# Kernel optimization log

Measured on AMD Instinct MI355X. Metric: run time of the kernel, lower is better.

The kernel has to match this reference:

```python
import jax, jax.numpy as jnp
import numpy as np
import math

EMBED_DIM = 2048
NUM_HEADS = 32
NUM_KV_HEADS = 8
HEAD_DIM = EMBED_DIM // NUM_HEADS  # 64
N_REP = NUM_HEADS // NUM_KV_HEADS  # 4
BATCH = 2
SEQ = 2048


def _rope_tables(seq_len, head_dim):
    # standard RoPE tables matching rotate_half convention (frequencies tiled twice)
    inv_freq = 1.0 / (10000.0 ** (np.arange(0, head_dim, 2, dtype=np.float32) / head_dim))
    t = np.arange(seq_len, dtype=np.float32)
    freqs = np.outer(t, inv_freq)                      # (seq, head_dim/2)
    emb = np.concatenate([freqs, freqs], axis=-1)      # (seq, head_dim)
    return jnp.asarray(np.cos(emb)), jnp.asarray(np.sin(emb))


def setup_inputs() -> dict:
    key = jax.random.key(0)
    ks = jax.random.split(key, 6)
    scale = 1.0 / math.sqrt(EMBED_DIM)
    x = jax.random.normal(ks[0], (BATCH, SEQ, EMBED_DIM), dtype=jnp.float32)
    wq = jax.random.normal(ks[1], (EMBED_DIM, EMBED_DIM), dtype=jnp.float32) * scale
    wk = jax.random.normal(ks[2], (NUM_KV_HEADS * HEAD_DIM, EMBED_DIM), dtype=jnp.float32) * scale
    wv = jax.random.normal(ks[3], (NUM_KV_HEADS * HEAD_DIM, EMBED_DIM), dtype=jnp.float32) * scale
    wo = jax.random.normal(ks[4], (EMBED_DIM, EMBED_DIM), dtype=jnp.float32) * scale
    freqs_cos, freqs_sin = _rope_tables(SEQ, HEAD_DIM)
    return {"x": x, "freqs_cos": freqs_cos, "freqs_sin": freqs_sin,
            "wq": wq, "wk": wk, "wv": wv, "wo": wo}


def _rotate_half(t):
    h = t.shape[-1] // 2
    return jnp.concatenate([-t[..., h:], t[..., :h]], axis=-1)


def reference(x, freqs_cos, freqs_sin, wq, wk, wv, wo):
    b, s, _ = x.shape
    # QKV projections (Linear with weight (out,in): y = x @ W^T)
    xq = (x @ wq.T).reshape(b, s, NUM_HEADS, HEAD_DIM).transpose(0, 2, 1, 3)     # (b,H,s,d)
    xk = (x @ wk.T).reshape(b, s, NUM_KV_HEADS, HEAD_DIM).transpose(0, 2, 1, 3)  # (b,Hkv,s,d)
    xv = (x @ wv.T).reshape(b, s, NUM_KV_HEADS, HEAD_DIM).transpose(0, 2, 1, 3)
    # RoPE: cos/sin (s,d) broadcast over (b,h,s,d)
    xq = xq * freqs_cos + _rotate_half(xq) * freqs_sin
    xk = xk * freqs_cos + _rotate_half(xk) * freqs_sin
    # GQA: repeat_interleave kv heads to match q heads
    xk = jnp.repeat(xk, N_REP, axis=1)  # (b,H,s,d)
    xv = jnp.repeat(xv, N_REP, axis=1)
    scores = jnp.einsum('bhqd,bhkd->bhqk', xq, xk) / math.sqrt(HEAD_DIM)
    causal = jnp.tril(jnp.ones((s, s), dtype=bool))
    scores = jnp.where(causal, scores, jnp.float32(-1e30))
    attn = jax.nn.softmax(scores, axis=-1)
    out = jnp.einsum('bhqk,bhkd->bhqd', attn, xv)        # (b,H,s,d)
    out = out.transpose(0, 2, 1, 3).reshape(b, s, EMBED_DIM)
    return out @ wo.T
```

## Files before the change

kernel.cpp:

```cpp
#include <hip/hip_runtime.h>

#define BATCH 2
#define SEQ 2048
#define EMBED 2048
#define NHEADS 32
#define NKV 8
#define HDIM 64
#define QKV_LD 3072
#define LOG2E 1.44269504088896f

typedef __attribute__((ext_vector_type(8))) short short8;
typedef __attribute__((ext_vector_type(4))) float f32x4;

__device__ inline float hw_exp2(float x) { return __builtin_amdgcn_exp2f(x); }

__device__ inline ushort f2bf(float f) {
  union { float f; unsigned u; } v{f};
  unsigned r = v.u + 0x7FFF + ((v.u >> 16) & 1);
  return (ushort)(r >> 16);
}
__device__ inline float bf2f(ushort u) {
  union { unsigned u; float f; } v{((unsigned)u) << 16};
  return v.f;
}
__device__ inline unsigned fbits(float f) {
  union { float f; unsigned u; } v{f};
  return v.u;
}

__device__ inline void gload16(const ushort* g, ushort* l) {
  __builtin_amdgcn_global_load_lds(
      (const __attribute__((address_space(1))) unsigned*)g,
      (__attribute__((address_space(3))) unsigned*)l, 16, 0, 0);
}

#define PHASE_BAR()                          \
  do {                                       \
    __builtin_amdgcn_sched_barrier(0);       \
    __builtin_amdgcn_s_barrier();            \
    __builtin_amdgcn_sched_barrier(0);       \
  } while (0)

__global__ __launch_bounds__(256) void cvt_all(const float* __restrict__ x,
                                               const float* __restrict__ wq,
                                               const float* __restrict__ wk,
                                               const float* __restrict__ wv,
                                               const float* __restrict__ wo,
                                               ushort* __restrict__ xb,
                                               ushort* __restrict__ wqkv,
                                               ushort* __restrict__ wob) {
  size_t e = (size_t)(blockIdx.x * blockDim.x + threadIdx.x) * 8;
  const float* src;
  ushort* dst;
  if (e < 8388608u) { src = x + e; dst = xb + e; }
  else if (e < 12582912u) { size_t o = e - 8388608u; src = wq + o; dst = wqkv + o; }
  else if (e < 13631488u) { size_t o = e - 12582912u; src = wk + o; dst = wqkv + 4194304u + o; }
  else if (e < 14680064u) { size_t o = e - 13631488u; src = wv + o; dst = wqkv + 5242880u + o; }
  else { size_t o = e - 14680064u; src = wo + o; dst = wob + o; }
  float4 v0 = ((const float4*)src)[0];
  float4 v1 = ((const float4*)src)[1];
  union { uint4 v; ushort u[8]; } pk;
  pk.u[0] = f2bf(v0.x); pk.u[1] = f2bf(v0.y); pk.u[2] = f2bf(v0.z); pk.u[3] = f2bf(v0.w);
  pk.u[4] = f2bf(v1.x); pk.u[5] = f2bf(v1.y); pk.u[6] = f2bf(v1.z); pk.u[7] = f2bf(v1.w);
  *(uint4*)dst = pk.v;
}

template <int BN, typename OutT>
__global__ __launch_bounds__(512) void gemm8p(const ushort* __restrict__ Ag,
                                              const ushort* __restrict__ Bg,
                                              OutT* __restrict__ C,
                                              int M, int N, int K) {
  constexpr int NF = BN / 64;
  __shared__ ushort As[2][2][256][32];
  __shared__ ushort Bs[2][2][BN][32];
  const int tid = threadIdx.x;
  const int lane = tid & 63, wave = tid >> 6;
  const int quad = lane >> 4, l16 = lane & 15;
  const int wm = wave >> 2, wn = wave & 3;
  const int m0 = blockIdx.y * 256, n0 = blockIdx.x * BN;
  const int NT = K >> 6;

  auto stA = [&](int Tn, int h) {
    const int r0 = h * 128 + wave * 16;
    const ushort* g = Ag + (size_t)(m0 + r0 + (lane >> 2)) * K + Tn * 64 + (lane & 3) * 8;
    gload16(g, &As[Tn & 1][0][r0][0]);
    gload16(g + 32, &As[Tn & 1][1][r0][0]);
  };
  auto stB = [&](int Tn, int h) {
    const int r0 = h * 128 + wave * 16;
    const ushort* g = Bg + (size_t)(n0 + r0 + (lane >> 2)) * K + Tn * 64 + (lane & 3) * 8;
    gload16(g, &Bs[Tn & 1][0][r0][0]);
    gload16(g + 32, &Bs[Tn & 1][1][r0][0]);
  };

  f32x4 acc[8][NF] = {};

  stA(0, 0); stA(0, 1);
  stB(0, 0);
  if constexpr (BN == 256) stB(0, 1);

  for (int T = 0; T < NT; ++T) {
    const int bf = T & 1;
    asm volatile("s_waitcnt vmcnt(0)" ::: "memory");
    PHASE_BAR();

    short8 bfr[NF][2];
#pragma unroll
    for (int nf = 0; nf < NF; nf++)
#pragma unroll
      for (int kk = 0; kk < 2; kk++)
        bfr[nf][kk] = *(short8*)&Bs[bf][kk][wn * (16 * NF) + nf * 16 + l16][quad * 8];

#pragma unroll
    for (int q = 0; q < 4; q++) {
      short8 afr[2][2];
#pragma unroll
      for (int mq = 0; mq < 2; mq++)
#pragma unroll
        for (int kk = 0; kk < 2; kk++)
          afr[mq][kk] = *(short8*)&As[bf][kk][wm * 128 + (2 * q + mq) * 16 + l16][quad * 8];

      if (T + 1 < NT) {
        if (q == 0) stA(T + 1, 0);
        else if (q == 1) stA(T + 1, 1);
        else if (q == 2) stB(T + 1, 0);
        else if constexpr (BN == 256) stB(T + 1, 1);
      }

      __builtin_amdgcn_s_setprio(1);
#pragma unroll
      for (int mq = 0; mq < 2; mq++)
#pragma unroll
        for (int nf = 0; nf < NF; nf++)
#pragma unroll
          for (int kk = 0; kk < 2; kk++)
            acc[2 * q + mq][nf] = __builtin_amdgcn_mfma_f32_16x16x32_bf16(
                afr[mq][kk], bfr[nf][kk], acc[2 * q + mq][nf], 0, 0, 0);
      __builtin_amdgcn_s_setprio(0);
      PHASE_BAR();
    }
  }

#pragma unroll
  for (int mf = 0; mf < 8; mf++) {
#pragma unroll
    for (int r = 0; r < 4; r++) {
      size_t rg = (size_t)(m0 + wm * 128 + mf * 16 + quad * 4 + r);
#pragma unroll
      for (int nf = 0; nf < NF; nf++) {
        int cg = n0 + wn * (16 * NF) + nf * 16 + l16;
        if constexpr (sizeof(OutT) == 2)
          C[rg * N + cg] = f2bf(acc[mf][nf][r]);
        else
          C[rg * N + cg] = acc[mf][nf][r];
      }
    }
  }
}

__global__ __launch_bounds__(256) void rope_qk(ushort* __restrict__ t,
                                               const float* __restrict__ fc,
                                               const float* __restrict__ fs,
                                               int total) {
  int idx = blockIdx.x * blockDim.x + threadIdx.x;
  if (idx >= total) return;
  int g = idx & 3;
  int hh = (idx >> 2) % 40;
  int tok = idx / 160;
  int s = tok & (SEQ - 1);
  float scale = (hh < 32) ? 0.125f * LOG2E : 1.0f;
  ushort* p = t + (size_t)tok * QKV_LD + hh * 64 + g * 8;
  union { uint4 v; ushort u[8]; } lo, hi, olo, ohi;
  lo.v = *(const uint4*)p;
  hi.v = *(const uint4*)(p + 32);
  const float* fcb = fc + s * HDIM + g * 8;
  const float* fsb = fs + s * HDIM + g * 8;
  float4 c0a = ((const float4*)fcb)[0], c0b = ((const float4*)fcb)[1];
  float4 s0a = ((const float4*)fsb)[0], s0b = ((const float4*)fsb)[1];
  float4 c1a = ((const float4*)(fcb + 32))[0], c1b = ((const float4*)(fcb + 32))[1];
  float4 s1a = ((const float4*)(fsb + 32))[0], s1b = ((const float4*)(fsb + 32))[1];
  float cc0[8] = {c0a.x, c0a.y, c0a.z, c0a.w, c0b.x, c0b.y, c0b.z, c0b.w};
  float ss0[8] = {s0a.x, s0a.y, s0a.z, s0a.w, s0b.x, s0b.y, s0b.z, s0b.w};
  float cc1[8] = {c1a.x, c1a.y, c1a.z, c1a.w, c1b.x, c1b.y, c1b.z, c1b.w};
  float ss1[8] = {s1a.x, s1a.y, s1a.z, s1a.w, s1b.x, s1b.y, s1b.z, s1b.w};
#pragma unroll
  for (int j = 0; j < 8; j++) {
    float x0 = bf2f(lo.u[j]), x1 = bf2f(hi.u[j]);
    olo.u[j] = f2bf((x0 * cc0[j] - x1 * ss0[j]) * scale);
    ohi.u[j] = f2bf((x1 * cc1[j] + x0 * ss1[j]) * scale);
  }
  *(uint4*)p = olo.v;
  *(uint4*)(p + 32) = ohi.v;
}

__global__ __launch_bounds__(256, 4) void attn_mfma(const ushort* __restrict__ QKV,
                                                    ushort* __restrict__ O) {
  __shared__ ushort Ks[64][72];
  __shared__ ushort Vt[64][72];
  __shared__ ushort Pw[4][16][72];
  const int tid = threadIdx.x;
  const int lane = tid & 63, wave = tid >> 6;
  const int quad = lane >> 4, l16 = lane & 15;

  const int bid = blockIdx.x;
  const int qq = bid >> 8;
  const int j4 = (bid >> 6) & 3;
  const int bh = bid & 63;
  const int qblk = (qq >> 1) * 8 + ((qq & 1) ? 7 - j4 : j4);

  const int b = bh >> 5, h = bh & 31, kh = h >> 2;
  const int ntiles = 2 * qblk + 2;
  const int wrow = qblk * 128 + wave * 32;

  short8 qf[2][2];
#pragma unroll
  for (int f = 0; f < 2; f++)
#pragma unroll
    for (int c = 0; c < 2; c++)
      qf[f][c] = *(const short8*)(QKV +
          (size_t)(b * SEQ + wrow + f * 16 + l16) * QKV_LD +
          h * HDIM + c * 32 + quad * 8);

  f32x4 o[2][4] = {};
  float m[2] = {-INFINITY, -INFINITY}, l[2] = {0.f, 0.f};

  const ushort* Kbase = QKV + (size_t)b * SEQ * QKV_LD + 2048 + kh * HDIM;
  const ushort* Vbase = Kbase + 512;
  const int kp = tid & 31, dg = tid >> 5;

  for (int t = 0; t < ntiles; t++) {
    const int k0 = t * 64;
    __syncthreads();
    {
      const float4* kpp = (const float4*)(Kbase + (size_t)(k0 + lane) * QKV_LD + wave * 16);
      float4 kv0 = kpp[0], kv1 = kpp[1];
      const uint4* va4 = (const uint4*)(Vbase + (size_t)(k0 + 2 * kp) * QKV_LD + dg * 8);
      const uint4* vb4 = (const uint4*)(Vbase + (size_t)(k0 + 2 * kp + 1) * QKV_LD + dg * 8);
      uint4 va = va4[0], vb = vb4[0];
      *(float4*)&Ks[lane][wave * 16] = kv0;
      *(float4*)&Ks[lane][wave * 16 + 8] = kv1;
      const unsigned* vaw = (const unsigned*)&va;
      const unsigned* vbw = (const unsigned*)&vb;
#pragma unroll
      for (int j = 0; j < 8; j++) {
        unsigned pk = (j & 1)
            ? __builtin_amdgcn_perm(vbw[j >> 1], vaw[j >> 1], 0x07060302)
            : __builtin_amdgcn_perm(vbw[j >> 1], vaw[j >> 1], 0x05040100);
        *(unsigned*)&Vt[dg * 8 + j][2 * kp] = pk;
      }
    }
    __syncthreads();

    if (k0 > wrow + 31) continue;
    const bool a0 = (k0 <= wrow + 15);

    f32x4 s0[4], s1[4];
    __builtin_amdgcn_s_setprio(1);
#pragma unroll
    for (int nt = 0; nt < 4; nt++) {
      short8 kf0 = *(short8*)&Ks[nt * 16 + l16][quad * 8];
      short8 kf1 = *(short8*)&Ks[nt * 16 + l16][32 + quad * 8];
      f32x4 z1 = {};
      z1 = __builtin_amdgcn_mfma_f32_16x16x32_bf16(kf0, qf[1][0], z1, 0, 0, 0);
      s1[nt] = __builtin_amdgcn_mfma_f32_16x16x32_bf16(kf1, qf[1][1], z1, 0, 0, 0);
      if (a0) {
        f32x4 z0 = {};
        z0 = __builtin_amdgcn_mfma_f32_16x16x32_bf16(kf0, qf[0][0], z0, 0, 0, 0);
        s0[nt] = __builtin_amdgcn_mfma_f32_16x16x32_bf16(kf1, qf[0][1], z0, 0, 0, 0);
      }
    }
    __builtin_amdgcn_s_setprio(0);

    if (k0 + 63 > wrow + 16) {
      const int lim1 = wrow + 16 + l16 - k0;
#pragma unroll
      for (int nt = 0; nt < 4; nt++)
#pragma unroll
        for (int r = 0; r < 4; r++)
          if (nt * 16 + quad * 4 + r > lim1) s1[nt][r] = -INFINITY;
    }
    if (a0 && k0 + 63 > wrow) {
      const int lim0 = wrow + l16 - k0;
#pragma unroll
      for (int nt = 0; nt < 4; nt++)
#pragma unroll
        for (int r = 0; r < 4; r++)
          if (nt * 16 + quad * 4 + r > lim0) s0[nt][r] = -INFINITY;
    }

    auto smx = [&](f32x4 (&s)[4], float& mm, float& ll, f32x4 (&oo)[4]) {
      float mx = s[0][0];
#pragma unroll
      for (int nt = 0; nt < 4; nt++)
#pragma unroll
        for (int r = 0; r < 4; r++) mx = fmaxf(mx, s[nt][r]);
      mx = fmaxf(mx, __shfl_xor(mx, 16));
      mx = fmaxf(mx, __shfl_xor(mx, 32));
      if (!__all(mx <= mm + 8.f)) {
        float mnew = fmaxf(mm, mx);
        float al = hw_exp2(mm - mnew);
        mm = mnew;
        ll *= al;
#pragma unroll
        for (int dt = 0; dt < 4; dt++)
#pragma unroll
          for (int r = 0; r < 4; r++) oo[dt][r] *= al;
      }
      float psum = 0.f;
#pragma unroll
      for (int nt = 0; nt < 4; nt++) {
        float p0 = hw_exp2(s[nt][0] - mm), p1 = hw_exp2(s[nt][1] - mm);
        float p2 = hw_exp2(s[nt][2] - mm), p3 = hw_exp2(s[nt][3] - mm);
        psum += (p0 + p1) + (p2 + p3);
        unsigned lo = __builtin_amdgcn_perm(fbits(p1), fbits(p0), 0x07060302);
        unsigned hi = __builtin_amdgcn_perm(fbits(p3), fbits(p2), 0x07060302);
        uint2 pk; pk.x = lo; pk.y = hi;
        *(uint2*)&Pw[wave][l16][nt * 16 + quad * 4] = pk;
      }
      psum += __shfl_xor(psum, 16);
      psum += __shfl_xor(psum, 32);
      ll += psum;
    };

    short8 pf00, pf01, pf10, pf11;
    if (a0) {
      smx(s0, m[0], l[0], o[0]);
      pf00 = *(short8*)&Pw[wave][l16][quad * 8];
      pf01 = *(short8*)&Pw[wave][l16][32 + quad * 8];
    }
    smx(s1, m[1], l[1], o[1]);
    pf10 = *(short8*)&Pw[wave][l16][quad * 8];
    pf11 = *(short8*)&Pw[wave][l16][32 + quad * 8];

    __builtin_amdgcn_s_setprio(1);
#pragma unroll
    for (int dt = 0; dt < 4; dt++) {
      short8 vf0 = *(short8*)&Vt[dt * 16 + l16][quad * 8];
      short8 vf1 = *(short8*)&Vt[dt * 16 + l16][32 + quad * 8];
      o[1][dt] = __builtin_amdgcn_mfma_f32_16x16x32_bf16(vf0, pf10, o[1][dt], 0, 0, 0);
      o[1][dt] = __builtin_amdgcn_mfma_f32_16x16x32_bf16(vf1, pf11, o[1][dt], 0, 0, 0);
      if (a0) {
        o[0][dt] = __builtin_amdgcn_mfma_f32_16x16x32_bf16(vf0, pf00, o[0][dt], 0, 0, 0);
        o[0][dt] = __builtin_amdgcn_mfma_f32_16x16x32_bf16(vf1, pf01, o[0][dt], 0, 0, 0);
      }
    }
    __builtin_amdgcn_s_setprio(0);
  }

#pragma unroll
  for (int f = 0; f < 2; f++) {
    float inv = 1.0f / l[f];
    size_t rowg = (size_t)(b * SEQ + wrow + f * 16 + l16) * EMBED + h * HDIM;
#pragma unroll
    for (int dt = 0; dt < 4; dt++) {
      ushort q0 = f2bf(o[f][dt][0] * inv), q1 = f2bf(o[f][dt][1] * inv);
      ushort q2 = f2bf(o[f][dt][2] * inv), q3 = f2bf(o[f][dt][3] * inv);
      uint2 pk;
      pk.x = (unsigned)q0 | ((unsigned)q1 << 16);
      pk.y = (unsigned)q2 | ((unsigned)q3 << 16);
      *(uint2*)&O[rowg + dt * 16 + quad * 4] = pk;
    }
  }
}

extern "C" void kernel_launch(void* const* d_in, const int* in_sizes, int n_in,
                              void* d_out, int out_size, void* d_ws, size_t ws_size,
                              hipStream_t stream) {
  const float* x = (const float*)d_in[0];
  const float* fcos = (const float*)d_in[1];
  const float* fsin = (const float*)d_in[2];
  const float* wq = (const float*)d_in[3];
  const float* wk = (const float*)d_in[4];
  const float* wv = (const float*)d_in[5];
  const float* wo = (const float*)d_in[6];
  float* out = (float*)d_out;

  const int M = BATCH * SEQ;
  ushort* ws = (ushort*)d_ws;
  ushort* xb = ws;
  ushort* wqkv = xb + (size_t)M * EMBED;
  ushort* wob = wqkv + (size_t)QKV_LD * EMBED;
  ushort* QKVb = wob + (size_t)EMBED * EMBED;
  ushort* Ab = QKVb + (size_t)M * QKV_LD;

  dim3 blk(256);
  cvt_all<<<9216, blk, 0, stream>>>(x, wq, wk, wv, wo, xb, wqkv, wob);

  gemm8p<256, ushort><<<dim3(QKV_LD / 256, M / 256), dim3(512), 0, stream>>>(xb, wqkv, QKVb, M, QKV_LD, EMBED);

  {
    int tot = M * 40 * 4;
    rope_qk<<<(tot + 255) / 256, blk, 0, stream>>>(QKVb, fcos, fsin, tot);
  }

  attn_mfma<<<dim3(1024), blk, 0, stream>>>(QKVb, Ab);

  gemm8p<128, float><<<dim3(EMBED / 128, M / 256), dim3(512), 0, stream>>>(Ab, wob, out, M, EMBED, EMBED);
}
```

Baseline: 317.6 us.

## Fuse RoPE into QKV GEMM epilogue and issue next-tile loads up front

Removes the standalone RoPE kernel by applying the rotation and Q scaling directly to the accumulators in the QKV GEMM epilogue, since each wave's 64 columns are exactly one head. This saves a full read and write pass over the Q/K region and one kernel launch. The GEMM main loop also now issues all next-tile global loads at the start of each K step instead of spreading them across the compute sub-phases. That changes latency hiding and may raise register or memory pressure.

```diff
diff --git a/kernel.cpp b/kernel.cpp
--- a/kernel.cpp
+++ b/kernel.cpp
@@ -65,10 +65,12 @@
   *(uint4*)dst = pk.v;
 }
 
-template <int BN, typename OutT>
+template <int BN, int MODE, typename OutT>
 __global__ __launch_bounds__(512) void gemm8p(const ushort* __restrict__ Ag,
                                               const ushort* __restrict__ Bg,
                                               OutT* __restrict__ C,
+                                              const float* __restrict__ fc,
+                                              const float* __restrict__ fs,
                                               int M, int N, int K) {
   constexpr int NF = BN / 64;
   __shared__ ushort As[2][2][256][32];
@@ -104,6 +106,12 @@
     asm volatile("s_waitcnt vmcnt(0)" ::: "memory");
     PHASE_BAR();
 
+    if (T + 1 < NT) {
+      stA(T + 1, 0); stA(T + 1, 1);
+      stB(T + 1, 0);
+      if constexpr (BN == 256) stB(T + 1, 1);
+    }
+
     short8 bfr[NF][2];
 #pragma unroll
     for (int nf = 0; nf < NF; nf++)
@@ -119,13 +127,6 @@
 #pragma unroll
         for (int kk = 0; kk < 2; kk++)
           afr[mq][kk] = *(short8*)&As[bf][kk][wm * 128 + (2 * q + mq) * 16 + l16][quad * 8];
-
-      if (T + 1 < NT) {
-        if (q == 0) stA(T + 1, 0);
-        else if (q == 1) stA(T + 1, 1);
-        else if (q == 2) stB(T + 1, 0);
-        else if constexpr (BN == 256) stB(T + 1, 1);
-      }
 
       __builtin_amdgcn_s_setprio(1);
 #pragma unroll
@@ -141,6 +142,35 @@
     }
   }
 
+  if constexpr (MODE == 1) {
+    if (n0 < 2560) {
+      const float scale = (n0 < 2048) ? 0.125f * LOG2E : 1.0f;
+      const int d0 = l16, d1 = l16 + 32;
+      const int e0 = l16 + 16, e1 = l16 + 48;
+#pragma unroll
+      for (int mf = 0; mf < 8; mf++) {
+#pragma unroll
+        for (int r = 0; r < 4; r++) {
+          size_t rg = (size_t)(m0 + wm * 128 + mf * 16 + quad * 4 + r);
+          int s = (int)(rg & (SEQ - 1));
+          const float* cb = fc + s * HDIM;
+          const float* sb = fs + s * HDIM;
+          float x0 = acc[mf][0][r], x2 = acc[mf][2][r];
+          float y1 = acc[mf][1][r], y3 = acc[mf][3][r];
+          float o0 = (x0 * cb[d0] - x2 * sb[d0]) * scale;
+          float o2 = (x2 * cb[d1] + x0 * sb[d1]) * scale;
+          float o1 = (y1 * cb[e0] - y3 * sb[e0]) * scale;
+          float o3 = (y3 * cb[e1] + y1 * sb[e1]) * scale;
+          ushort* Cr = (ushort*)C + rg * N + n0 + wn * 64 + l16;
+          Cr[0]  = f2bf(o0);
+          Cr[16] = f2bf(o1);
+          Cr[32] = f2bf(o2);
+          Cr[48] = f2bf(o3);
+        }
+      }
+      return;
+    }
+  }
 #pragma unroll
   for (int mf = 0; mf < 8; mf++) {
 #pragma unroll
@@ -156,41 +186,6 @@
       }
     }
   }
-}
-
-__global__ __launch_bounds__(256) void rope_qk(ushort* __restrict__ t,
-                                               const float* __restrict__ fc,
-                                               const float* __restrict__ fs,
-                                               int total) {
-  int idx = blockIdx.x * blockDim.x + threadIdx.x;
-  if (idx >= total) return;
-  int g = idx & 3;
-  int hh = (idx >> 2) % 40;
-  int tok = idx / 160;
-  int s = tok & (SEQ - 1);
-  float scale = (hh < 32) ? 0.125f * LOG2E : 1.0f;
-  ushort* p = t + (size_t)tok * QKV_LD + hh * 64 + g * 8;
-  union { uint4 v; ushort u[8]; } lo, hi, olo, ohi;
-  lo.v = *(const uint4*)p;
-  hi.v = *(const uint4*)(p + 32);
-  const float* fcb = fc + s * HDIM + g * 8;
-  const float* fsb = fs + s * HDIM + g * 8;
-  float4 c0a = ((const float4*)fcb)[0], c0b = ((const float4*)fcb)[1];
-  float4 s0a = ((const float4*)fsb)[0], s0b = ((const float4*)fsb)[1];
-  float4 c1a = ((const float4*)(fcb + 32))[0], c1b = ((const float4*)(fcb + 32))[1];
-  float4 s1a = ((const float4*)(fsb + 32))[0], s1b = ((const float4*)(fsb + 32))[1];
-  float cc0[8] = {c0a.x, c0a.y, c0a.z, c0a.w, c0b.x, c0b.y, c0b.z, c0b.w};
-  float ss0[8] = {s0a.x, s0a.y, s0a.z, s0a.w, s0b.x, s0b.y, s0b.z, s0b.w};
-  float cc1[8] = {c1a.x, c1a.y, c1a.z, c1a.w, c1b.x, c1b.y, c1b.z, c1b.w};
-  float ss1[8] = {s1a.x, s1a.y, s1a.z, s1a.w, s1b.x, s1b.y, s1b.z, s1b.w};
-#pragma unroll
-  for (int j = 0; j < 8; j++) {
-    float x0 = bf2f(lo.u[j]), x1 = bf2f(hi.u[j]);
-    olo.u[j] = f2bf((x0 * cc0[j] - x1 * ss0[j]) * scale);
-    ohi.u[j] = f2bf((x1 * cc1[j] + x0 * ss1[j]) * scale);
-  }
-  *(uint4*)p = olo.v;
-  *(uint4*)(p + 32) = ohi.v;
 }
 
 __global__ __launch_bounds__(256, 4) void attn_mfma(const ushort* __restrict__ QKV,
@@ -386,14 +381,11 @@
   dim3 blk(256);
   cvt_all<<<9216, blk, 0, stream>>>(x, wq, wk, wv, wo, xb, wqkv, wob);
 
-  gemm8p<256, ushort><<<dim3(QKV_LD / 256, M / 256), dim3(512), 0, stream>>>(xb, wqkv, QKVb, M, QKV_LD, EMBED);
-
-  {
-    int tot = M * 40 * 4;
-    rope_qk<<<(tot + 255) / 256, blk, 0, stream>>>(QKVb, fcos, fsin, tot);
-  }
+  gemm8p<256, 1, ushort><<<dim3(QKV_LD / 256, M / 256), dim3(512), 0, stream>>>(
+      xb, wqkv, QKVb, fcos, fsin, M, QKV_LD, EMBED);
 
   attn_mfma<<<dim3(1024), blk, 0, stream>>>(QKVb, Ab);
 
-  gemm8p<128, float><<<dim3(EMBED / 128, M / 256), dim3(512), 0, stream>>>(Ab, wob, out, M, EMBED, EMBED);
-}
+  gemm8p<128, 0, float><<<dim3(EMBED / 128, M / 256), dim3(512), 0, stream>>>(
+      Ab, wob, out, nullptr, nullptr, M, EMBED, EMBED);
+}
```

Measured after the change: 337.0 us. 6.1% more time.
